# Kernel optimization log

Hardware: AMD Instinct MI355X
Metric: run time of the kernel (lower is better)

The kernel has to match this reference:

```python
import jax, jax.numpy as jnp
import numpy as np

N = 100000          # nodes of type 'note'
E = 800000          # edges per relation
D = 128             # in_feat == hidden_channels
NUM_LAYERS = 3
NUM_REL = 3         # onset, consecutive, during


def setup_inputs() -> dict:
    key = jax.random.key(0)
    ks = jax.random.split(key, 12)
    inp = {
        "x": jax.random.normal(ks[0], (N, D), dtype=jnp.float32),
        "edge_index_onset": jax.random.randint(ks[1], (2, E), 0, N, dtype=jnp.int64),
        "edge_index_consecutive": jax.random.randint(ks[2], (2, E), 0, N, dtype=jnp.int64),
        "edge_index_during": jax.random.randint(ks[3], (2, E), 0, N, dtype=jnp.int64),
        # hop masks: sorted node hops (seeds first), edge hops in [0, num_layers]
        "node_mask": jnp.sort(jax.random.randint(ks[4], (N,), 0, NUM_LAYERS + 1, dtype=jnp.int64)),
        "edge_mask_onset": jax.random.randint(ks[5], (E,), 0, NUM_LAYERS + 1, dtype=jnp.int64),
        "edge_mask_consecutive": jax.random.randint(ks[6], (E,), 0, NUM_LAYERS + 1, dtype=jnp.int64),
        "edge_mask_during": jax.random.randint(ks[7], (E,), 0, NUM_LAYERS + 1, dtype=jnp.int64),
        # SAGEConv weights per (layer, relation): lin_l (with bias) on aggregated
        # neighbor mean, lin_r (no bias) on root features.
        "W_l": jax.random.normal(ks[8], (NUM_LAYERS, NUM_REL, D, D), dtype=jnp.float32) / np.sqrt(D),
        "b_l": jnp.zeros((NUM_LAYERS, NUM_REL, D), dtype=jnp.float32),
        "W_r": jax.random.normal(ks[9], (NUM_LAYERS, NUM_REL, D, D), dtype=jnp.float32) / np.sqrt(D),
    }
    return inp


def _hetero_sage_forward(x, edge_indices, node_mask, edge_masks, W_l, b_l, W_r):
    h = x
    for i in range(NUM_LAYERS):
        layer = NUM_LAYERS - i  # trim_to_layer(layer=num_layers - i, ...)
        nvalid = node_mask <= layer                      # [N] kept nodes this layer
        out = jnp.zeros((N, D), dtype=h.dtype)
        for t in range(NUM_REL):
            src, dst = edge_indices[t][0], edge_indices[t][1]
            evalid = (edge_masks[t] <= layer).astype(h.dtype)  # [E] kept edges
            msg = h[src] * evalid[:, None]                     # gather + mask  [E, D]
            agg = jax.ops.segment_sum(msg, dst, num_segments=N)          # [N, D]
            cnt = jax.ops.segment_sum(evalid, dst, num_segments=N)       # [N]
            mean = agg / jnp.maximum(cnt, 1.0)[:, None]
            # SAGEConv: lin_l(mean) + lin_r(x_root); HeteroConv aggr='sum' over relations
            out = out + mean @ W_l[i, t].T + b_l[i, t] + h @ W_r[i, t].T
        h = jnp.where(nvalid[:, None], jax.nn.relu(out), 0.0)
    return h


def reference(x, edge_index_onset, edge_index_consecutive, edge_index_during,
              node_mask, edge_mask_onset, edge_mask_consecutive, edge_mask_during,
              W_l, b_l, W_r):
    edge_indices = (edge_index_onset, edge_index_consecutive, edge_index_during)
    edge_masks = (edge_mask_onset, edge_mask_consecutive, edge_mask_during)
    return _hetero_sage_forward(x, edge_indices, node_mask, edge_masks, W_l, b_l, W_r)
```

## Files before the change

### kernel.cpp

```cpp
#include <hip/hip_runtime.h>

#define N_NODES 100000
#define N_EDGES 800000
#define D 128
#define SCAN_N (4 * N_NODES)
#define SCAN_TOTAL (3 * SCAN_N)
#define SCAN_CHUNK 2048
#define SCAN_BLOCKS 586
#define SCAN_PAD (SCAN_BLOCKS * SCAN_CHUNK)

typedef _Float16 f16x8 __attribute__((ext_vector_type(8)));
typedef _Float16 f16x4 __attribute__((ext_vector_type(4)));
typedef float f32x4 __attribute__((ext_vector_type(4)));

#define MFMA_F16(a, b, c) __builtin_amdgcn_mfma_f32_16x16x32_f16((a), (b), (c), 0, 0, 0)

#define CONV_BLOCKS 12500
#define COUNT_BLOCKS 9375
#define PREPW_BLOCKS 768

__global__ __launch_bounds__(256) void prep_all(
    const float* __restrict__ x, _Float16* __restrict__ h,
    const int* __restrict__ ei0, const int* __restrict__ ei1, const int* __restrict__ ei2,
    const int* __restrict__ em0, const int* __restrict__ em1, const int* __restrict__ em2,
    int* __restrict__ cnt2, const float* __restrict__ W_l, const float* __restrict__ W_r,
    const float* __restrict__ b_l, _Float16* __restrict__ whi, float* __restrict__ bsum) {
    int b = blockIdx.x;
    int tid = threadIdx.x;
    if (b < CONV_BLOCKS) {
        int idx = b * 256 + tid;
        float4 v = reinterpret_cast<const float4*>(x)[idx];
        f16x4 o = {(_Float16)v.x, (_Float16)v.y, (_Float16)v.z, (_Float16)v.w};
        reinterpret_cast<f16x4*>(h)[idx] = o;
    } else if (b < CONV_BLOCKS + COUNT_BLOCKS) {
        int e = (b - CONV_BLOCKS) * 256 + tid;
        int r = e / N_EDGES;
        int el = e - r * N_EDGES;
        const int* ei = (r == 0) ? ei0 : (r == 1) ? ei1 : ei2;
        const int* em = (r == 0) ? em0 : (r == 1) ? em1 : em2;
        int dst = ei[N_EDGES + el];
        int m = em[el];
        atomicAdd(&cnt2[(size_t)r * SCAN_N + dst * 4 + m], 1);
    } else {
        int idx = (b - CONV_BLOCKS - COUNT_BLOCKS) * 256 + tid;
        if (idx < 3 * 4 * 16384) {
            int i = idx / (4 * 16384);
            int rem = idx % (4 * 16384);
            int slot = rem / 16384;
            int ok = rem % 16384;
            float v;
            if (slot < 3) {
                v = W_l[(size_t)(i * 3 + slot) * 16384 + ok];
            } else {
                const float* base = W_r + (size_t)i * 3 * 16384;
                v = base[ok] + base[16384 + ok] + base[2 * 16384 + ok];
            }
            whi[idx] = (_Float16)v;
        }
        if (idx < 3 * 128) {
            int i = idx / 128, o = idx % 128;
            const float* bb = b_l + (size_t)i * 3 * 128;
            bsum[idx] = bb[o] + bb[128 + o] + bb[256 + o];
        }
    }
}

__global__ __launch_bounds__(256) void scan_part(const int* __restrict__ cnt2,
                                                 int* __restrict__ bsums) {
    int tid = threadIdx.x;
    size_t base = (size_t)blockIdx.x * SCAN_CHUNK + tid * 8;
    int4 v0 = *reinterpret_cast<const int4*>(cnt2 + base);
    int4 v1 = *reinterpret_cast<const int4*>(cnt2 + base + 4);
    int s = v0.x + v0.y + v0.z + v0.w + v1.x + v1.y + v1.z + v1.w;
    __shared__ int red[256];
    red[tid] = s;
    __syncthreads();
    for (int off = 128; off > 0; off >>= 1) {
        if (tid < off) red[tid] += red[tid + off];
        __syncthreads();
    }
    if (tid == 0) bsums[blockIdx.x] = red[0];
}

__global__ __launch_bounds__(1024) void scan_tops(int* __restrict__ bsums) {
    __shared__ int s[1024];
    int tid = threadIdx.x;
    int v = (tid < SCAN_BLOCKS) ? bsums[tid] : 0;
    s[tid] = v;
    __syncthreads();
    for (int off = 1; off < 1024; off <<= 1) {
        int x = s[tid];
        int add = (tid >= off) ? s[tid - off] : 0;
        __syncthreads();
        s[tid] = x + add;
        __syncthreads();
    }
    if (tid < SCAN_BLOCKS) bsums[tid] = s[tid] - v;
}

__global__ __launch_bounds__(256) void scan_out(const int* __restrict__ cnt2,
                                                const int* __restrict__ bsums,
                                                int* __restrict__ bnd) {
    int tid = threadIdx.x;
    size_t base = (size_t)blockIdx.x * SCAN_CHUNK + tid * 8;
    int4 v0 = *reinterpret_cast<const int4*>(cnt2 + base);
    int4 v1 = *reinterpret_cast<const int4*>(cnt2 + base + 4);
    int l[8] = {v0.x, v0.y, v0.z, v0.w, v1.x, v1.y, v1.z, v1.w};
    int ts = l[0] + l[1] + l[2] + l[3] + l[4] + l[5] + l[6] + l[7];
    __shared__ int s[256];
    s[tid] = ts;
    __syncthreads();
    for (int off = 1; off < 256; off <<= 1) {
        int x = s[tid];
        int add = (tid >= off) ? s[tid - off] : 0;
        __syncthreads();
        s[tid] = x + add;
        __syncthreads();
    }
    int run = bsums[blockIdx.x] + s[tid] - ts;
    int o[8];
#pragma unroll
    for (int j = 0; j < 8; j++) {
        o[j] = run;
        run += l[j];
    }
    int4 o0 = {o[0], o[1], o[2], o[3]};
    int4 o1 = {o[4], o[5], o[6], o[7]};
    *reinterpret_cast<int4*>(bnd + base) = o0;
    *reinterpret_cast<int4*>(bnd + base + 4) = o1;
}

__global__ __launch_bounds__(256) void fill3(
    const int* __restrict__ ei0, const int* __restrict__ ei1, const int* __restrict__ ei2,
    const int* __restrict__ em0, const int* __restrict__ em1, const int* __restrict__ em2,
    const int* __restrict__ bnd, int* __restrict__ fill2, int* __restrict__ packed) {
    int e = blockIdx.x * 256 + threadIdx.x;
    int r = e / N_EDGES;
    int el = e - r * N_EDGES;
    const int* ei = (r == 0) ? ei0 : (r == 1) ? ei1 : ei2;
    const int* em = (r == 0) ? em0 : (r == 1) ? em1 : em2;
    int dst = ei[N_EDGES + el];
    int src = ei[el];
    int m = em[el];
    int gbk = r * SCAN_N + dst * 4 + m;
    int pos = bnd[gbk] + atomicAdd(&fill2[gbk], 1);
    packed[pos] = src * D;
}

__global__ __launch_bounds__(256, 4) void fused_layer(
    const _Float16* __restrict__ h_in, const int* __restrict__ bnd,
    const int* __restrict__ packed, const _Float16* __restrict__ Whi,
    const float* __restrict__ bias, const int* __restrict__ node_mask, int layer,
    _Float16* __restrict__ h_out, float* __restrict__ out_f32) {
    __shared__ __align__(16) _Float16 smean[3][32][136];
    int tid = threadIdx.x;
    int wid = tid >> 6;
    int lane = tid & 63;
    int row0 = blockIdx.x * 32;
    int g = lane >> 4;
    int l = lane & 15;

    const _Float16* hbase = h_in + l * 8;
#pragma unroll 1
    for (int it = 0; it < 6; it++) {
        int t = wid * 24 + it * 4 + g;
        int r = t >> 5;
        int n = t & 31;
        const int* B = bnd + (size_t)r * SCAN_N + (row0 + n) * 4;
        int beg = B[0];
        int end = B[layer + 1];
        int deg = end - beg;
        f16x8 acc = (f16x8)(_Float16)0;
#pragma unroll 1
        for (int e4 = beg & ~3; e4 < end; e4 += 4) {
            int4 s4 = *reinterpret_cast<const int4*>(packed + e4);
            if (e4 >= beg && e4 + 4 <= end) {
                f16x8 v0 = *reinterpret_cast<const f16x8*>(hbase + (size_t)(uint)s4.x);
                f16x8 v1 = *reinterpret_cast<const f16x8*>(hbase + (size_t)(uint)s4.y);
                f16x8 v2 = *reinterpret_cast<const f16x8*>(hbase + (size_t)(uint)s4.z);
                f16x8 v3 = *reinterpret_cast<const f16x8*>(hbase + (size_t)(uint)s4.w);
                acc += v0;
                acc += v1;
                acc += v2;
                acc += v3;
            } else {
                int ss[4] = {s4.x, s4.y, s4.z, s4.w};
#pragma unroll
                for (int j = 0; j < 4; j++) {
                    int e = e4 + j;
                    if (e >= beg && e < end)
                        acc += *reinterpret_cast<const f16x8*>(hbase + (size_t)(uint)ss[j]);
                }
            }
        }
        float inv = 1.f / fmaxf((float)deg, 1.f);
        f16x8 mv;
#pragma unroll
        for (int k = 0; k < 8; k++) mv[k] = (_Float16)((float)acc[k] * inv);
        *reinterpret_cast<f16x8*>(&smean[r][n][l * 8]) = mv;
    }
    __syncthreads();

    int colbase = wid * 32;
    int ln15 = lane & 15;
    int lg = lane >> 4;
    f32x4 acc[2][2] = {};

#pragma unroll
    for (int p = 0; p < 4; p++) {
        const _Float16* Whp = Whi + (size_t)p * 16384 + (size_t)colbase * D;
#pragma unroll
        for (int ks = 0; ks < 4; ks++) {
            int kof = ks * 32 + lg * 8;
            f16x8 a0f, a1f;
            if (p < 3) {
                a0f = *reinterpret_cast<const f16x8*>(&smean[p][ln15][kof]);
                a1f = *reinterpret_cast<const f16x8*>(&smean[p][16 + ln15][kof]);
            } else {
                a0f = *reinterpret_cast<const f16x8*>(h_in + (size_t)(row0 + ln15) * D + kof);
                a1f = *reinterpret_cast<const f16x8*>(h_in + (size_t)(row0 + 16 + ln15) * D + kof);
            }
            f16x8 bh0 = *reinterpret_cast<const f16x8*>(Whp + (size_t)ln15 * D + kof);
            f16x8 bh1 = *reinterpret_cast<const f16x8*>(Whp + (size_t)(16 + ln15) * D + kof);
            acc[0][0] = MFMA_F16(a0f, bh0, acc[0][0]);
            acc[0][1] = MFMA_F16(a0f, bh1, acc[0][1]);
            acc[1][0] = MFMA_F16(a1f, bh0, acc[1][0]);
            acc[1][1] = MFMA_F16(a1f, bh1, acc[1][1]);
        }
    }

#pragma unroll
    for (int r = 0; r < 2; r++)
#pragma unroll
        for (int j = 0; j < 4; j++) {
            int row = row0 + r * 16 + lg * 4 + j;
            bool valid = node_mask[row] <= layer;
#pragma unroll
            for (int cc = 0; cc < 2; cc++) {
                int col = colbase + cc * 16 + ln15;
                float v = acc[r][cc][j] + bias[col];
                v = valid ? fmaxf(v, 0.f) : 0.f;
                if (out_f32)
                    out_f32[(size_t)row * D + col] = v;
                else
                    h_out[(size_t)row * D + col] = (_Float16)v;
            }
        }
}

extern "C" void kernel_launch(void* const* d_in, const int* in_sizes, int n_in,
                              void* d_out, int out_size, void* d_ws, size_t ws_size,
                              hipStream_t stream) {
    const float* x = (const float*)d_in[0];
    const int* ei0 = (const int*)d_in[1];
    const int* ei1 = (const int*)d_in[2];
    const int* ei2 = (const int*)d_in[3];
    const int* node_mask = (const int*)d_in[4];
    const int* em0 = (const int*)d_in[5];
    const int* em1 = (const int*)d_in[6];
    const int* em2 = (const int*)d_in[7];
    const float* W_l = (const float*)d_in[8];
    const float* b_l = (const float*)d_in[9];
    const float* W_r = (const float*)d_in[10];

    _Float16* hA = (_Float16*)d_ws;
    _Float16* hB = hA + (size_t)N_NODES * D;
    _Float16* whi = hB + (size_t)N_NODES * D;
    float* bsum = (float*)(whi + 3 * 4 * 16384);
    int* cnt2 = (int*)(bsum + 3 * 128);
    int* fill2 = cnt2 + SCAN_PAD;
    int* bsums = fill2 + SCAN_TOTAL;
    int* bnd = bsums + 640;
    int* packed = bnd + SCAN_PAD;

    hipMemsetAsync(cnt2, 0, (size_t)(SCAN_PAD + SCAN_TOTAL) * sizeof(int), stream);

    prep_all<<<CONV_BLOCKS + COUNT_BLOCKS + PREPW_BLOCKS, 256, 0, stream>>>(
        x, hA, ei0, ei1, ei2, em0, em1, em2, cnt2, W_l, W_r, b_l, whi, bsum);
    scan_part<<<SCAN_BLOCKS, 256, 0, stream>>>(cnt2, bsums);
    scan_tops<<<1, 1024, 0, stream>>>(bsums);
    scan_out<<<SCAN_BLOCKS, 256, 0, stream>>>(cnt2, bsums, bnd);
    fill3<<<COUNT_BLOCKS, 256, 0, stream>>>(ei0, ei1, ei2, em0, em1, em2, bnd, fill2, packed);

    _Float16* hin = hA;
    _Float16* hout = hB;
    for (int i = 0; i < 3; i++) {
        int layer = 3 - i;
        float* of = (i == 2) ? (float*)d_out : nullptr;
        fused_layer<<<N_NODES / 32, 256, 0, stream>>>(
            hin, bnd, packed, whi + (size_t)i * 4 * 16384,
            bsum + (size_t)i * 128, node_mask, layer, hout, of);
        _Float16* tmp = hin; hin = hout; hout = tmp;
    }
}
```

Baseline: 711.1 us.

## Skip masked node tiles and software-pipeline the neighbor gather loop

Blocks whose first node already exceeds the layer cutoff write zeros and exit early. This relies on node_mask being sorted, so every later node in the block is also masked. Per-node aggregation is skipped for masked nodes. The gather loop is split into a scalar head, an aligned int4 body and a scalar tail, and the body prefetches the next four rows before summing the current ones, to overlap memory latency. The masked nodes' smean entries are left uninitialized, which is harmless only if the epilogue masks those rows. The pipelined body also keeps more registers live.

```diff
diff --git a/kernel.cpp b/kernel.cpp
--- a/kernel.cpp
+++ b/kernel.cpp
@@ -157,6 +157,22 @@
     int wid = tid >> 6;
     int lane = tid & 63;
     int row0 = blockIdx.x * 32;
+
+    if (node_mask[row0] > layer) {
+        if (out_f32) {
+            f32x4 z = {0.f, 0.f, 0.f, 0.f};
+            f32x4* o = reinterpret_cast<f32x4*>(out_f32 + (size_t)row0 * D);
+#pragma unroll
+            for (int k = 0; k < 4; k++) o[tid + k * 256] = z;
+        } else {
+            f16x8 z = (f16x8)(_Float16)0;
+            f16x8* o = reinterpret_cast<f16x8*>(h_out + (size_t)row0 * D);
+#pragma unroll
+            for (int k = 0; k < 2; k++) o[tid + k * 256] = z;
+        }
+        return;
+    }
+
     int g = lane >> 4;
     int l = lane & 15;
 
@@ -166,32 +182,38 @@
         int t = wid * 24 + it * 4 + g;
         int r = t >> 5;
         int n = t & 31;
+        if (node_mask[row0 + n] > layer) continue;
         const int* B = bnd + (size_t)r * SCAN_N + (row0 + n) * 4;
         int beg = B[0];
         int end = B[layer + 1];
         int deg = end - beg;
         f16x8 acc = (f16x8)(_Float16)0;
+        int abeg = (beg + 3) & ~3;
+        int aend = end & ~3;
+        if (abeg >= aend) {
+            for (int e = beg; e < end; e++)
+                acc += *reinterpret_cast<const f16x8*>(hbase + (size_t)(uint)packed[e]);
+        } else {
+            for (int e = beg; e < abeg; e++)
+                acc += *reinterpret_cast<const f16x8*>(hbase + (size_t)(uint)packed[e]);
+            int4 s = *reinterpret_cast<const int4*>(packed + abeg);
+            f16x8 r0 = *reinterpret_cast<const f16x8*>(hbase + (size_t)(uint)s.x);
+            f16x8 r1 = *reinterpret_cast<const f16x8*>(hbase + (size_t)(uint)s.y);
+            f16x8 r2 = *reinterpret_cast<const f16x8*>(hbase + (size_t)(uint)s.z);
+            f16x8 r3 = *reinterpret_cast<const f16x8*>(hbase + (size_t)(uint)s.w);
 #pragma unroll 1
-        for (int e4 = beg & ~3; e4 < end; e4 += 4) {
-            int4 s4 = *reinterpret_cast<const int4*>(packed + e4);
-            if (e4 >= beg && e4 + 4 <= end) {
-                f16x8 v0 = *reinterpret_cast<const f16x8*>(hbase + (size_t)(uint)s4.x);
-                f16x8 v1 = *reinterpret_cast<const f16x8*>(hbase + (size_t)(uint)s4.y);
-                f16x8 v2 = *reinterpret_cast<const f16x8*>(hbase + (size_t)(uint)s4.z);
-                f16x8 v3 = *reinterpret_cast<const f16x8*>(hbase + (size_t)(uint)s4.w);
-                acc += v0;
-                acc += v1;
-                acc += v2;
-                acc += v3;
-            } else {
-                int ss[4] = {s4.x, s4.y, s4.z, s4.w};
-#pragma unroll
-                for (int j = 0; j < 4; j++) {
-                    int e = e4 + j;
-                    if (e >= beg && e < end)
-                        acc += *reinterpret_cast<const f16x8*>(hbase + (size_t)(uint)ss[j]);
-                }
+            for (int e4 = abeg + 4; e4 < aend; e4 += 4) {
+                int4 sn = *reinterpret_cast<const int4*>(packed + e4);
+                f16x8 n0 = *reinterpret_cast<const f16x8*>(hbase + (size_t)(uint)sn.x);
+                f16x8 n1 = *reinterpret_cast<const f16x8*>(hbase + (size_t)(uint)sn.y);
+                f16x8 n2 = *reinterpret_cast<const f16x8*>(hbase + (size_t)(uint)sn.z);
+                f16x8 n3 = *reinterpret_cast<const f16x8*>(hbase + (size_t)(uint)sn.w);
+                acc += (r0 + r1) + (r2 + r3);
+                r0 = n0; r1 = n1; r2 = n2; r3 = n3;
             }
+            acc += (r0 + r1) + (r2 + r3);
+            for (int e = aend; e < end; e++)
+                acc += *reinterpret_cast<const f16x8*>(hbase + (size_t)(uint)packed[e]);
         }
         float inv = 1.f / fmaxf((float)deg, 1.f);
         f16x8 mv;
```

Result: faster. 676.9 us (-4.8%).
